# Optimization experiments

Measured on AMD Instinct MI355X. Metric: run time of the kernel, lower is better.

## Reference

```python
import jax, jax.numpy as jnp
import numpy as np

D = 256   # feature_dim
NQ = 512  # num query keypoints
NK = 512  # num key/value keypoints


def setup_inputs() -> dict:
    key = jax.random.key(0)
    ks = jax.random.split(key, 10)
    def w(k, shape, fan_in):
        return jax.random.normal(k, shape, dtype=jnp.float32) / np.sqrt(fan_in)
    inp = {
        "x": jax.random.normal(ks[0], (1, D, NQ), dtype=jnp.float32),
        "source": jax.random.normal(ks[1], (1, D, NK), dtype=jnp.float32),
        # MLPAttention score MLP: Conv1d(2D->D,k=1), ReLU, Conv1d(D->1,k=1)
        "w1": w(ks[2], (D, 2 * D), 2 * D),
        "b1": w(ks[3], (D,), 2 * D),
        "w2": w(ks[4], (1, D), D),
        "b2": w(ks[5], (1,), D),
        # outer MLP: Conv1d(2D->2D,k=1), ReLU, Conv1d(2D->D,k=1) with zero bias init
        "wa": w(ks[6], (2 * D, 2 * D), 2 * D),
        "ba": w(ks[7], (2 * D,), 2 * D),
        "wb": w(ks[8], (D, 2 * D), 2 * D),
        "bb": jnp.zeros((D,), dtype=jnp.float32),
    }
    return inp


def reference(x, source, w1, b1, w2, b2, wa, ba, wb, bb):
    d = x.shape[1]
    q = x[0]       # [D, nq]
    k = source[0]  # [D, nk]
    # cat((q broadcast over nk, k broadcast over nq)) then Conv1d(2D->D) is
    # equivalent to splitting w1 into query/key halves and broadcasting:
    w1q, w1k = w1[:, :d], w1[:, d:]
    aq = w1q @ q + b1[:, None]                       # [D, nq]
    ak = w1k @ k                                     # [D, nk]
    h = jax.nn.relu(aq[:, :, None] + ak[:, None, :])  # [D, nq, nk]
    scores = (jnp.einsum('d,dnm->nm', w2[0], h) + b2[0])[None]  # [1, nq, nk]
    prob = jax.nn.softmax(scores, axis=-1)
    message = jnp.einsum('bnm,bdm->bdn', prob, source)  # [1, D, nq]
    # outer MLP on cat([x, message], channel dim)
    cat = jnp.concatenate([x, message], axis=1)         # [1, 2D, nq]
    h2 = jax.nn.relu(jnp.einsum('oc,bcn->bon', wa, cat) + ba[None, :, None])
    y = jnp.einsum('oc,bcn->bon', wb, h2) + bb[None, :, None]  # [1, D, nq]
    return (y, scores)
```

## Files before the change

kernel.cpp:

```cpp
#include <hip/hip_runtime.h>
#include <hip/hip_bf16.h>

#define DD 256
#define NN 512

typedef __attribute__((ext_vector_type(8))) short short8;
typedef __attribute__((ext_vector_type(4))) float floatx4;

__device__ __forceinline__ unsigned short f2bf(float f) {
  unsigned u = __float_as_uint(f);
  u += 0x7FFFu + ((u >> 16) & 1u);
  return (unsigned short)(u >> 16);
}
__device__ __forceinline__ unsigned pack2(float a, float b) {
  return (unsigned)f2bf(a) | ((unsigned)f2bf(b) << 16);
}
__device__ __forceinline__ float bflo(unsigned u) { return __uint_as_float(u << 16); }
__device__ __forceinline__ float bfhi(unsigned u) { return __uint_as_float(u & 0xFFFF0000u); }

__device__ __forceinline__ short8 ldfrag(const unsigned short* __restrict__ base,
                                         int row, int ld, int k, int lane) {
  return *(const short8*)(base + (row + (lane & 15)) * ld + k + ((lane >> 4) << 3));
}

template <int NF>
__device__ __forceinline__ void acc_zero(floatx4 acc[NF]) {
#pragma unroll
  for (int i = 0; i < NF; ++i) {
    acc[i][0] = 0.f; acc[i][1] = 0.f; acc[i][2] = 0.f; acc[i][3] = 0.f;
  }
}

template <int NF>
__device__ __forceinline__ void ksplit_combine(floatx4 acc[NF], float* red,
                                               int wave, int lane) {
  const int W = 16 * NF;
  const int col = lane & 15;
  const int q = lane >> 4;
  if (wave > 0) {
    float* base = red + (wave - 1) * 16 * W;
#pragma unroll
    for (int nf = 0; nf < NF; ++nf)
#pragma unroll
      for (int r = 0; r < 4; ++r)
        base[(q * 4 + r) * W + nf * 16 + col] = acc[nf][r];
  }
  __syncthreads();
  if (wave == 0) {
#pragma unroll
    for (int nf = 0; nf < NF; ++nf)
#pragma unroll
      for (int r = 0; r < 4; ++r) {
        const int idx = (q * 4 + r) * W + nf * 16 + col;
        acc[nf][r] += red[idx] + red[16 * W + idx] + red[32 * W + idx];
      }
  }
}

template <int NF, bool COLBIAS, bool ROWBIAS, bool RELU, bool OUTBF>
__device__ __forceinline__ void gemm_epi(floatx4 acc[NF],
    const float* __restrict__ bias, void* __restrict__ C, int ldc,
    int m0, int n0, int lane) {
  const int col = lane & 15;
  const int q = lane >> 4;
#pragma unroll
  for (int nf = 0; nf < NF; ++nf) {
    const int n = n0 + nf * 16 + col;
    const float cb = COLBIAS ? bias[n] : 0.0f;
#pragma unroll
    for (int r = 0; r < 4; ++r) {
      const int m = m0 + q * 4 + r;
      float v = acc[nf][r] + cb + (ROWBIAS ? bias[m] : 0.0f);
      if (RELU) v = fmaxf(v, 0.0f);
      if (OUTBF) ((unsigned short*)C)[m * ldc + n] = f2bf(v);
      else       ((float*)C)[m * ldc + n] = v;
    }
  }
}

__global__ __launch_bounds__(256) void prep_kernel(
    const float* __restrict__ x, const float* __restrict__ src,
    const float* __restrict__ w1, const float* __restrict__ wa,
    const float* __restrict__ wb, const float* __restrict__ bb,
    unsigned short* __restrict__ w1b, unsigned short* __restrict__ wab,
    unsigned short* __restrict__ wbb, unsigned short* __restrict__ srcb,
    unsigned short* __restrict__ xT, unsigned short* __restrict__ srcT,
    float* __restrict__ y) {
  const int bid = blockIdx.x;
  const int tid = threadIdx.x;
  if (bid < 640) {
    const float* in; unsigned short* out; int off;
    if (bid < 128)      { in = w1;  out = w1b; off = bid; }
    else if (bid < 384) { in = wa;  out = wab; off = bid - 128; }
    else if (bid < 512) { in = wb;  out = wbb; off = bid - 384; }
    else                { in = src; out = srcb; off = bid - 512; }
    const int i = off * 1024 + tid * 4;
    const float4 v = *(const float4*)(in + i);
    *(uint2*)(out + i) = make_uint2(pack2(v.x, v.y), pack2(v.z, v.w));
  } else if (bid < 896) {
    __shared__ float tile[32][33];
    const int b = bid - 640;
    const float* in = (b >> 7) ? src : x;
    unsigned short* out = (b >> 7) ? srcT : xT;
    const int t = b & 127;
    const int n0 = (t >> 3) * 32;
    const int d0 = (t & 7) * 32;
    const int tx = tid & 31, ty = tid >> 5;
#pragma unroll
    for (int i = ty; i < 32; i += 8)
      tile[i][tx] = in[(d0 + i) * NN + n0 + tx];
    __syncthreads();
#pragma unroll
    for (int i = ty; i < 32; i += 8)
      out[(n0 + i) * DD + d0 + tx] = f2bf(tile[tx][i]);
  } else {
    const int i = (bid - 896) * 1024 + tid * 4;
    const float bv = bb[i >> 9];
    float4 o; o.x = bv; o.y = bv; o.z = bv; o.w = bv;
    *(float4*)(y + i) = o;
  }
}

__global__ __launch_bounds__(256) void qks_kernel(
    const unsigned short* __restrict__ w1b, const unsigned short* __restrict__ xT,
    const unsigned short* __restrict__ srcT, const float* __restrict__ b1,
    const float* __restrict__ w2, const float* __restrict__ b2,
    float* __restrict__ sc) {
  __shared__ __align__(16) unsigned short aqs[256][36];
  __shared__ __align__(16) unsigned short aks[256][36];
  __shared__ __align__(16) float part[4][32][32];
  __shared__ float w2s[DD];

  const int tid = threadIdx.x;
  const int lane = tid & 63;
  const int wave = tid >> 6;
  const int n0 = blockIdx.x * 32;
  const int m0 = blockIdx.y * 32;

  w2s[tid] = w2[tid];

  {
    const int col = lane & 15, q = lane >> 4;
#pragma unroll
    for (int j = 0; j < 8; ++j) {
      const int jid = wave * 8 + j;
      const int z = jid >> 4;
      const int d0t = (jid & 15) * 16;
      const unsigned short* BT = z ? srcT : xT;
      const int tok0 = z ? m0 : n0;
      floatx4 acc[2]; acc_zero<2>(acc);
#pragma unroll
      for (int kc = 0; kc < 8; ++kc) {
        const int c0 = kc * 32;
        short8 a = ldfrag(w1b, d0t, NN, z * 256 + c0, lane);
#pragma unroll
        for (int nf = 0; nf < 2; ++nf) {
          short8 b = ldfrag(BT, tok0 + nf * 16, DD, c0, lane);
          acc[nf] = __builtin_amdgcn_mfma_f32_16x16x32_bf16(a, b, acc[nf], 0, 0, 0);
        }
      }
#pragma unroll
      for (int nf = 0; nf < 2; ++nf)
#pragma unroll
        for (int r = 0; r < 4; ++r) {
          const int d = d0t + q * 4 + r;
          float v = acc[nf][r] + (z ? 0.0f : b1[d]);
          (z ? aks : aqs)[d][nf * 16 + col] = f2bf(v);
        }
    }
  }
  __syncthreads();

  {
    const int nq = lane & 7;
    const int mq = lane >> 3;
    float s[4][4];
#pragma unroll
    for (int i = 0; i < 4; ++i)
#pragma unroll
      for (int j = 0; j < 4; ++j) s[i][j] = 0.f;

    const int dbeg = wave * 64;
    for (int dd = dbeg; dd < dbeg + 64; ++dd) {
      const uint2 aw = *(const uint2*)&aqs[dd][nq * 4];
      const uint2 kw = *(const uint2*)&aks[dd][mq * 4];
      const float w = w2s[dd];
      float a[4] = {bflo(aw.x), bfhi(aw.x), bflo(aw.y), bfhi(aw.y)};
      float k[4] = {bflo(kw.x), bfhi(kw.x), bflo(kw.y), bfhi(kw.y)};
#pragma unroll
      for (int i = 0; i < 4; ++i)
#pragma unroll
        for (int j = 0; j < 4; ++j)
          s[i][j] += w * fmaxf(a[i] + k[j], 0.f);
    }
#pragma unroll
    for (int i = 0; i < 4; ++i)
#pragma unroll
      for (int j = 0; j < 4; ++j)
        part[wave][nq * 4 + i][mq * 4 + j] = s[i][j];
  }
  __syncthreads();

  {
    const int n = tid >> 3;
    const int mg = (tid & 7) * 4;
    float4 p0 = *(const float4*)&part[0][n][mg];
    float4 p1 = *(const float4*)&part[1][n][mg];
    float4 p2 = *(const float4*)&part[2][n][mg];
    float4 p3 = *(const float4*)&part[3][n][mg];
    const float bv = b2[0];
    float4 o;
    o.x = p0.x + p1.x + p2.x + p3.x + bv;
    o.y = p0.y + p1.y + p2.y + p3.y + bv;
    o.z = p0.z + p1.z + p2.z + p3.z + bv;
    o.w = p0.w + p1.w + p2.w + p3.w + bv;
    *(float4*)&sc[(n0 + n) * NN + m0 + mg] = o;
  }
}

__global__ __launch_bounds__(256) void msgT_kernel(
    const float* __restrict__ sc, const unsigned short* __restrict__ srcb,
    unsigned short* __restrict__ msgTb) {
  __shared__ unsigned short Ap[16][520];
  __shared__ float red[1536];
  __shared__ float smax[16][16];
  __shared__ float ssum[16][16];
  __shared__ float rst[16][2];

  const int tid = threadIdx.x;
  const int lane = tid & 63;
  const int wave = tid >> 6;
  const int n0 = blockIdx.y * 16;
  const int d0 = blockIdx.x * 32;

  const int r = tid >> 4;
  const int c = tid & 15;
  float4 v[8];
  const float* rp = sc + (n0 + r) * NN + c * 4;
#pragma unroll
  for (int i = 0; i < 8; ++i) v[i] = *(const float4*)(rp + i * 64);

  float mx = -3.0e38f;
#pragma unroll
  for (int i = 0; i < 8; ++i)
    mx = fmaxf(mx, fmaxf(fmaxf(v[i].x, v[i].y), fmaxf(v[i].z, v[i].w)));
  smax[r][c] = mx;
  __syncthreads();
  if (c == 0) {
    float m2 = smax[r][0];
#pragma unroll
    for (int i = 1; i < 16; ++i) m2 = fmaxf(m2, smax[r][i]);
    rst[r][0] = m2;
  }
  __syncthreads();
  mx = rst[r][0];

  float sum = 0.f;
#pragma unroll
  for (int i = 0; i < 8; ++i) {
    v[i].x = __expf(v[i].x - mx); v[i].y = __expf(v[i].y - mx);
    v[i].z = __expf(v[i].z - mx); v[i].w = __expf(v[i].w - mx);
    sum += v[i].x + v[i].y + v[i].z + v[i].w;
  }
  ssum[r][c] = sum;
  __syncthreads();
  if (c == 0) {
    float s2 = ssum[r][0];
#pragma unroll
    for (int i = 1; i < 16; ++i) s2 += ssum[r][i];
    rst[r][1] = s2;
  }
  __syncthreads();
  const float inv = 1.0f / rst[r][1];
#pragma unroll
  for (int i = 0; i < 8; ++i) {
    *(unsigned*)&Ap[r][c * 4 + i * 64]     = pack2(v[i].x * inv, v[i].y * inv);
    *(unsigned*)&Ap[r][c * 4 + i * 64 + 2] = pack2(v[i].z * inv, v[i].w * inv);
  }
  __syncthreads();

  floatx4 acc[2]; acc_zero<2>(acc);
  const int k0w = wave * 128;
  const int arow = lane & 15;
  const int koff = (lane >> 4) << 3;
#pragma unroll
  for (int k = 0; k < 128; k += 32) {
    short8 a = *(const short8*)&Ap[arow][k0w + k + koff];
#pragma unroll
    for (int nf = 0; nf < 2; ++nf) {
      short8 b = ldfrag(srcb, d0 + nf * 16, NN, k0w + k, lane);
      acc[nf] = __builtin_amdgcn_mfma_f32_16x16x32_bf16(a, b, acc[nf], 0, 0, 0);
    }
  }
  ksplit_combine<2>(acc, red, wave, lane);
  if (wave == 0)
    gemm_epi<2, false, false, false, true>(acc, nullptr, msgTb, DD, n0, d0, lane);
}

__global__ __launch_bounds__(256) void h2y_kernel(
    const unsigned short* __restrict__ xT, const unsigned short* __restrict__ msgTb,
    const unsigned short* __restrict__ wab, const unsigned short* __restrict__ wbb,
    const float* __restrict__ ba, float* __restrict__ y) {
  __shared__ __align__(16) unsigned short h2L[16][144];

  const int tid = threadIdx.x;
  const int lane = tid & 63;
  const int wave = tid >> 6;
  const int nt = blockIdx.x >> 2;
  const int qh = blockIdx.x & 3;
  const int n0g = nt * 16;
  const int o0 = qh * 128;

  {
    floatx4 acc[2]; acc_zero<2>(acc);
    const int ow = o0 + wave * 32;
#pragma unroll
    for (int kc = 0; kc < 16; ++kc) {
      const int c0 = kc * 32;
      short8 a = (c0 < 256) ? ldfrag(xT, n0g, DD, c0, lane)
                            : ldfrag(msgTb, n0g, DD, c0 - 256, lane);
#pragma unroll
      for (int nf = 0; nf < 2; ++nf) {
        short8 b = ldfrag(wab, ow + nf * 16, NN, c0, lane);
        acc[nf] = __builtin_amdgcn_mfma_f32_16x16x32_bf16(a, b, acc[nf], 0, 0, 0);
      }
    }
    const int col = lane & 15, q = lane >> 4;
#pragma unroll
    for (int nf = 0; nf < 2; ++nf) {
      const int ol = wave * 32 + nf * 16 + col;
      const float cb = ba[o0 + ol];
#pragma unroll
      for (int r = 0; r < 4; ++r)
        h2L[q * 4 + r][ol] = f2bf(fmaxf(acc[nf][r] + cb, 0.f));
    }
  }
  __syncthreads();

  {
    const int brow = lane & 15;
    const int koff = (lane >> 4) << 3;
    const int col = lane & 15, q = lane >> 4;
#pragma unroll
    for (int t = 0; t < 4; ++t) {
      const int o2t = wave * 64 + t * 16;
      floatx4 acc;
      acc[0] = 0.f; acc[1] = 0.f; acc[2] = 0.f; acc[3] = 0.f;
#pragma unroll
      for (int kc = 0; kc < 4; ++kc) {
        short8 a = ldfrag(wbb, o2t, NN, o0 + kc * 32, lane);
        short8 b = *(const short8*)&h2L[brow][kc * 32 + koff];
        acc = __builtin_amdgcn_mfma_f32_16x16x32_bf16(a, b, acc, 0, 0, 0);
      }
#pragma unroll
      for (int r = 0; r < 4; ++r)
        atomicAdd(&y[(o2t + q * 4 + r) * NN + n0g + col], acc[r]);
    }
  }
}

extern "C" void kernel_launch(void* const* d_in, const int* in_sizes, int n_in,
                              void* d_out, int out_size, void* d_ws, size_t ws_size,
                              hipStream_t stream) {
  (void)in_sizes; (void)n_in; (void)out_size; (void)ws_size;

  const float* x   = (const float*)d_in[0];
  const float* src = (const float*)d_in[1];
  const float* w1  = (const float*)d_in[2];
  const float* b1  = (const float*)d_in[3];
  const float* w2  = (const float*)d_in[4];
  const float* b2  = (const float*)d_in[5];
  const float* wa  = (const float*)d_in[6];
  const float* ba  = (const float*)d_in[7];
  const float* wb  = (const float*)d_in[8];
  const float* bb  = (const float*)d_in[9];

  float* y_out  = (float*)d_out;
  float* sc_out = (float*)d_out + 131072;

  char* ws = (char*)d_ws;
  unsigned short* w1b   = (unsigned short*)(ws);
  unsigned short* wab   = (unsigned short*)(ws + (256 << 10));
  unsigned short* wbb   = (unsigned short*)(ws + (768 << 10));
  unsigned short* srcb  = (unsigned short*)(ws + (1024 << 10));
  unsigned short* xT    = (unsigned short*)(ws + (1280 << 10));
  unsigned short* srcT  = (unsigned short*)(ws + (1536 << 10));
  unsigned short* msgTb = (unsigned short*)(ws + (1792 << 10));

  prep_kernel<<<1024, 256, 0, stream>>>(x, src, w1, wa, wb, bb,
                                        w1b, wab, wbb, srcb, xT, srcT, y_out);
  qks_kernel<<<dim3(16, 16), 256, 0, stream>>>(w1b, xT, srcT, b1, w2, b2, sc_out);
  msgT_kernel<<<dim3(8, 32), 256, 0, stream>>>(sc_out, srcb, msgTb);
  h2y_kernel<<<128, 256, 0, stream>>>(xT, msgTb, wab, wbb, ba, y_out);
}
```

Measured before the change: 122.7 us.

## Drop bf16 prep pass; convert fp32 inputs on the fly and split aq/ak from scores

Removes the separate prep kernel that converted weights and inputs to bf16 and transposed them. The GEMM kernels now read fp32 directly and convert to bf16 in registers (ldfrag_f32), or transpose through LDS. aq/ak are now computed once by a dedicated kernel into fp32 workspace instead of being recomputed per score tile, and the scores kernel reads them back. The aim is to cut redundant aq/ak recomputation and the extra conversion traffic. In exchange, the weights are re-read and re-converted in fp32 by many blocks, which means more global bytes per fragment and strided LDS transposes.

```diff
diff --git a/kernel.cpp b/kernel.cpp
--- a/kernel.cpp
+++ b/kernel.cpp
@@ -15,12 +15,33 @@
 __device__ __forceinline__ unsigned pack2(float a, float b) {
   return (unsigned)f2bf(a) | ((unsigned)f2bf(b) << 16);
 }
-__device__ __forceinline__ float bflo(unsigned u) { return __uint_as_float(u << 16); }
-__device__ __forceinline__ float bfhi(unsigned u) { return __uint_as_float(u & 0xFFFF0000u); }
 
 __device__ __forceinline__ short8 ldfrag(const unsigned short* __restrict__ base,
                                          int row, int ld, int k, int lane) {
   return *(const short8*)(base + (row + (lane & 15)) * ld + k + ((lane >> 4) << 3));
+}
+
+__device__ __forceinline__ short8 ldfrag_f32(const float* __restrict__ base,
+                                             int row, int ld, int k, int lane) {
+  const float* p = base + (row + (lane & 15)) * ld + k + ((lane >> 4) << 3);
+  const float4 v0 = *(const float4*)p;
+  const float4 v1 = *(const float4*)(p + 4);
+  short8 r;
+  r[0] = (short)f2bf(v0.x); r[1] = (short)f2bf(v0.y);
+  r[2] = (short)f2bf(v0.z); r[3] = (short)f2bf(v0.w);
+  r[4] = (short)f2bf(v1.x); r[5] = (short)f2bf(v1.y);
+  r[6] = (short)f2bf(v1.z); r[7] = (short)f2bf(v1.w);
+  return r;
+}
+
+__device__ __forceinline__ short8 ldfragT_lds(const float* __restrict__ xs, int ldxs,
+                                              int nrow, int k, int lane) {
+  const int n = nrow + (lane & 15);
+  const int kk = k + ((lane >> 4) << 3);
+  short8 r;
+#pragma unroll
+  for (int j = 0; j < 8; ++j) r[j] = (short)f2bf(xs[(kk + j) * ldxs + n]);
+  return r;
 }
 
 template <int NF>
@@ -78,148 +99,103 @@
   }
 }
 
-__global__ __launch_bounds__(256) void prep_kernel(
+__global__ __launch_bounds__(256) void aqak_kernel(
     const float* __restrict__ x, const float* __restrict__ src,
-    const float* __restrict__ w1, const float* __restrict__ wa,
-    const float* __restrict__ wb, const float* __restrict__ bb,
-    unsigned short* __restrict__ w1b, unsigned short* __restrict__ wab,
-    unsigned short* __restrict__ wbb, unsigned short* __restrict__ srcb,
-    unsigned short* __restrict__ xT, unsigned short* __restrict__ srcT,
-    float* __restrict__ y) {
-  const int bid = blockIdx.x;
+    const float* __restrict__ w1, const float* __restrict__ b1,
+    const float* __restrict__ bb,
+    float* __restrict__ aq, float* __restrict__ ak, float* __restrict__ y) {
+  __shared__ float xs[256][33];
+  __shared__ float red[1536];
+
   const int tid = threadIdx.x;
-  if (bid < 640) {
-    const float* in; unsigned short* out; int off;
-    if (bid < 128)      { in = w1;  out = w1b; off = bid; }
-    else if (bid < 384) { in = wa;  out = wab; off = bid - 128; }
-    else if (bid < 512) { in = wb;  out = wbb; off = bid - 384; }
-    else                { in = src; out = srcb; off = bid - 512; }
-    const int i = off * 1024 + tid * 4;
-    const float4 v = *(const float4*)(in + i);
-    *(uint2*)(out + i) = make_uint2(pack2(v.x, v.y), pack2(v.z, v.w));
-  } else if (bid < 896) {
-    __shared__ float tile[32][33];
-    const int b = bid - 640;
-    const float* in = (b >> 7) ? src : x;
-    unsigned short* out = (b >> 7) ? srcT : xT;
-    const int t = b & 127;
-    const int n0 = (t >> 3) * 32;
-    const int d0 = (t & 7) * 32;
-    const int tx = tid & 31, ty = tid >> 5;
-#pragma unroll
-    for (int i = ty; i < 32; i += 8)
-      tile[i][tx] = in[(d0 + i) * NN + n0 + tx];
-    __syncthreads();
-#pragma unroll
-    for (int i = ty; i < 32; i += 8)
-      out[(n0 + i) * DD + d0 + tx] = f2bf(tile[tx][i]);
-  } else {
-    const int i = (bid - 896) * 1024 + tid * 4;
-    const float bv = bb[i >> 9];
-    float4 o; o.x = bv; o.y = bv; o.z = bv; o.w = bv;
-    *(float4*)(y + i) = o;
-  }
-}
-
-__global__ __launch_bounds__(256) void qks_kernel(
-    const unsigned short* __restrict__ w1b, const unsigned short* __restrict__ xT,
-    const unsigned short* __restrict__ srcT, const float* __restrict__ b1,
+  const int z = blockIdx.z;
+
+  if (z == 2) {
+    const int o = blockIdx.y * 16 + blockIdx.x;
+    const float bv = bb[o];
+    float2 v; v.x = bv; v.y = bv;
+    *(float2*)&y[o * NN + tid * 2] = v;
+    return;
+  }
+
+  const int lane = tid & 63;
+  const int wave = tid >> 6;
+  const int m0 = blockIdx.y * 16;
+  const int n0 = blockIdx.x * 32;
+  const float* in = z ? src : x;
+
+#pragma unroll
+  for (int p = 0; p < 8; ++p) {
+    const int d = p * 32 + (tid >> 3);
+    const int c4 = (tid & 7) * 4;
+    const float4 v = *(const float4*)&in[d * NN + n0 + c4];
+    xs[d][c4 + 0] = v.x; xs[d][c4 + 1] = v.y;
+    xs[d][c4 + 2] = v.z; xs[d][c4 + 3] = v.w;
+  }
+  __syncthreads();
+
+  floatx4 acc[2]; acc_zero<2>(acc);
+#pragma unroll
+  for (int kc = 0; kc < 2; ++kc) {
+    const int kl = wave * 64 + kc * 32;
+    short8 a = ldfrag_f32(w1, m0, NN, z * 256 + kl, lane);
+#pragma unroll
+    for (int nf = 0; nf < 2; ++nf) {
+      short8 b = ldfragT_lds(&xs[0][0], 33, nf * 16, kl, lane);
+      acc[nf] = __builtin_amdgcn_mfma_f32_16x16x32_bf16(a, b, acc[nf], 0, 0, 0);
+    }
+  }
+  ksplit_combine<2>(acc, red, wave, lane);
+  if (wave == 0) {
+    if (z == 0) gemm_epi<2, false, true, false, false>(acc, b1, aq, NN, m0, n0, lane);
+    else        gemm_epi<2, false, false, false, false>(acc, nullptr, ak, NN, m0, n0, lane);
+  }
+}
+
+__global__ __launch_bounds__(256) void scores_kernel(
+    const float* __restrict__ aq, const float* __restrict__ ak,
     const float* __restrict__ w2, const float* __restrict__ b2,
     float* __restrict__ sc) {
-  __shared__ __align__(16) unsigned short aqs[256][36];
-  __shared__ __align__(16) unsigned short aks[256][36];
-  __shared__ __align__(16) float part[4][32][32];
+  __shared__ float aqs[128][32];
+  __shared__ float aks[128][32];
   __shared__ float w2s[DD];
 
   const int tid = threadIdx.x;
-  const int lane = tid & 63;
-  const int wave = tid >> 6;
   const int n0 = blockIdx.x * 32;
   const int m0 = blockIdx.y * 32;
+  const int tn = tid & 31;
+  const int tm4 = (tid >> 5) * 4;
 
   w2s[tid] = w2[tid];
 
-  {
-    const int col = lane & 15, q = lane >> 4;
-#pragma unroll
-    for (int j = 0; j < 8; ++j) {
-      const int jid = wave * 8 + j;
-      const int z = jid >> 4;
-      const int d0t = (jid & 15) * 16;
-      const unsigned short* BT = z ? srcT : xT;
-      const int tok0 = z ? m0 : n0;
-      floatx4 acc[2]; acc_zero<2>(acc);
-#pragma unroll
-      for (int kc = 0; kc < 8; ++kc) {
-        const int c0 = kc * 32;
-        short8 a = ldfrag(w1b, d0t, NN, z * 256 + c0, lane);
-#pragma unroll
-        for (int nf = 0; nf < 2; ++nf) {
-          short8 b = ldfrag(BT, tok0 + nf * 16, DD, c0, lane);
-          acc[nf] = __builtin_amdgcn_mfma_f32_16x16x32_bf16(a, b, acc[nf], 0, 0, 0);
-        }
-      }
-#pragma unroll
-      for (int nf = 0; nf < 2; ++nf)
-#pragma unroll
-        for (int r = 0; r < 4; ++r) {
-          const int d = d0t + q * 4 + r;
-          float v = acc[nf][r] + (z ? 0.0f : b1[d]);
-          (z ? aks : aqs)[d][nf * 16 + col] = f2bf(v);
-        }
-    }
-  }
-  __syncthreads();
-
-  {
-    const int nq = lane & 7;
-    const int mq = lane >> 3;
-    float s[4][4];
-#pragma unroll
-    for (int i = 0; i < 4; ++i)
-#pragma unroll
-      for (int j = 0; j < 4; ++j) s[i][j] = 0.f;
-
-    const int dbeg = wave * 64;
-    for (int dd = dbeg; dd < dbeg + 64; ++dd) {
-      const uint2 aw = *(const uint2*)&aqs[dd][nq * 4];
-      const uint2 kw = *(const uint2*)&aks[dd][mq * 4];
-      const float w = w2s[dd];
-      float a[4] = {bflo(aw.x), bfhi(aw.x), bflo(aw.y), bfhi(aw.y)};
-      float k[4] = {bflo(kw.x), bfhi(kw.x), bflo(kw.y), bfhi(kw.y)};
-#pragma unroll
-      for (int i = 0; i < 4; ++i)
-#pragma unroll
-        for (int j = 0; j < 4; ++j)
-          s[i][j] += w * fmaxf(a[i] + k[j], 0.f);
-    }
-#pragma unroll
-    for (int i = 0; i < 4; ++i)
-#pragma unroll
-      for (int j = 0; j < 4; ++j)
-        part[wave][nq * 4 + i][mq * 4 + j] = s[i][j];
-  }
-  __syncthreads();
-
-  {
-    const int n = tid >> 3;
-    const int mg = (tid & 7) * 4;
-    float4 p0 = *(const float4*)&part[0][n][mg];
-    float4 p1 = *(const float4*)&part[1][n][mg];
-    float4 p2 = *(const float4*)&part[2][n][mg];
-    float4 p3 = *(const float4*)&part[3][n][mg];
-    const float bv = b2[0];
-    float4 o;
-    o.x = p0.x + p1.x + p2.x + p3.x + bv;
-    o.y = p0.y + p1.y + p2.y + p3.y + bv;
-    o.z = p0.z + p1.z + p2.z + p3.z + bv;
-    o.w = p0.w + p1.w + p2.w + p3.w + bv;
-    *(float4*)&sc[(n0 + n) * NN + m0 + mg] = o;
-  }
+  float s0 = 0.f, s1 = 0.f, s2 = 0.f, s3 = 0.f;
+  for (int d0 = 0; d0 < DD; d0 += 128) {
+    __syncthreads();
+#pragma unroll
+    for (int k = 0; k < 16; ++k) {
+      const int idx = k * 256 + tid;
+      const int r = idx >> 5, cc = idx & 31;
+      aqs[r][cc] = aq[(d0 + r) * NN + n0 + cc];
+      aks[r][cc] = ak[(d0 + r) * NN + m0 + cc];
+    }
+    __syncthreads();
+    for (int dd = 0; dd < 128; ++dd) {
+      const float w = w2s[d0 + dd];
+      const float a = aqs[dd][tn];
+      const float4 akv = *(const float4*)&aks[dd][tm4];
+      s0 += w * fmaxf(a + akv.x, 0.f);
+      s1 += w * fmaxf(a + akv.y, 0.f);
+      s2 += w * fmaxf(a + akv.z, 0.f);
+      s3 += w * fmaxf(a + akv.w, 0.f);
+    }
+  }
+  const float bv = b2[0];
+  float4 o; o.x = s0 + bv; o.y = s1 + bv; o.z = s2 + bv; o.w = s3 + bv;
+  *(float4*)&sc[(n0 + tn) * NN + m0 + tm4] = o;
 }
 
 __global__ __launch_bounds__(256) void msgT_kernel(
-    const float* __restrict__ sc, const unsigned short* __restrict__ srcb,
+    const float* __restrict__ sc, const float* __restrict__ srcf,
     unsigned short* __restrict__ msgTb) {
   __shared__ unsigned short Ap[16][520];
   __shared__ float red[1536];
@@ -288,7 +264,7 @@
     short8 a = *(const short8*)&Ap[arow][k0w + k + koff];
 #pragma unroll
     for (int nf = 0; nf < 2; ++nf) {
-      short8 b = ldfrag(srcb, d0 + nf * 16, NN, k0w + k, lane);
+      short8 b = ldfrag_f32(srcf, d0 + nf * 16, NN, k0w + k, lane);
       acc[nf] = __builtin_amdgcn_mfma_f32_16x16x32_bf16(a, b, acc[nf], 0, 0, 0);
     }
   }
@@ -298,10 +274,11 @@
 }
 
 __global__ __launch_bounds__(256) void h2y_kernel(
-    const unsigned short* __restrict__ xT, const unsigned short* __restrict__ msgTb,
-    const unsigned short* __restrict__ wab, const unsigned short* __restrict__ wbb,
+    const float* __restrict__ x, const unsigned short* __restrict__ msgTb,
+    const float* __restrict__ waf, const float* __restrict__ wbf,
     const float* __restrict__ ba, float* __restrict__ y) {
-  __shared__ __align__(16) unsigned short h2L[16][144];
+  __shared__ float xs[256][17];
+  __shared__ __align__(16) unsigned short h2L[16][152];
 
   const int tid = threadIdx.x;
   const int lane = tid & 63;
@@ -311,17 +288,25 @@
   const int n0g = nt * 16;
   const int o0 = qh * 128;
 
+#pragma unroll
+  for (int p = 0; p < 16; ++p) {
+    const int d = p * 16 + (tid >> 4);
+    const int n = tid & 15;
+    xs[d][n] = x[d * NN + n0g + n];
+  }
+  __syncthreads();
+
   {
     floatx4 acc[2]; acc_zero<2>(acc);
     const int ow = o0 + wave * 32;
 #pragma unroll
     for (int kc = 0; kc < 16; ++kc) {
       const int c0 = kc * 32;
-      short8 a = (c0 < 256) ? ldfrag(xT, n0g, DD, c0, lane)
+      short8 a = (c0 < 256) ? ldfragT_lds(&xs[0][0], 17, 0, c0, lane)
                             : ldfrag(msgTb, n0g, DD, c0 - 256, lane);
 #pragma unroll
       for (int nf = 0; nf < 2; ++nf) {
-        short8 b = ldfrag(wab, ow + nf * 16, NN, c0, lane);
+        short8 b = ldfrag_f32(waf, ow + nf * 16, NN, c0, lane);
         acc[nf] = __builtin_amdgcn_mfma_f32_16x16x32_bf16(a, b, acc[nf], 0, 0, 0);
       }
     }
@@ -348,7 +333,7 @@
       acc[0] = 0.f; acc[1] = 0.f; acc[2] = 0.f; acc[3] = 0.f;
 #pragma unroll
       for (int kc = 0; kc < 4; ++kc) {
-        short8 a = ldfrag(wbb, o2t, NN, o0 + kc * 32, lane);
+        short8 a = ldfrag_f32(wbf, o2t, NN, o0 + kc * 32, lane);
         short8 b = *(const short8*)&h2L[brow][kc * 32 + koff];
         acc = __builtin_amdgcn_mfma_f32_16x16x32_bf16(a, b, acc, 0, 0, 0);
       }
@@ -379,17 +364,12 @@
   float* sc_out = (float*)d_out + 131072;
 
   char* ws = (char*)d_ws;
-  unsigned short* w1b   = (unsigned short*)(ws);
-  unsigned short* wab   = (unsigned short*)(ws + (256 << 10));
-  unsigned short* wbb   = (unsigned short*)(ws + (768 << 10));
-  unsigned short* srcb  = (unsigned short*)(ws + (1024 << 10));
-  unsigned short* xT    = (unsigned short*)(ws + (1280 << 10));
-  unsigned short* srcT  = (unsigned short*)(ws + (1536 << 10));
-  unsigned short* msgTb = (unsigned short*)(ws + (1792 << 10));
-
-  prep_kernel<<<1024, 256, 0, stream>>>(x, src, w1, wa, wb, bb,
-                                        w1b, wab, wbb, srcb, xT, srcT, y_out);
-  qks_kernel<<<dim3(16, 16), 256, 0, stream>>>(w1b, xT, srcT, b1, w2, b2, sc_out);
-  msgT_kernel<<<dim3(8, 32), 256, 0, stream>>>(sc_out, srcb, msgTb);
-  h2y_kernel<<<128, 256, 0, stream>>>(xT, msgTb, wab, wbb, ba, y_out);
-}
+  float*          aq    = (float*)(ws);
+  float*          ak    = (float*)(ws + (512 << 10));
+  unsigned short* msgTb = (unsigned short*)(ws + (1024 << 10));
+
+  aqak_kernel<<<dim3(16, 16, 3), 256, 0, stream>>>(x, src, w1, b1, bb, aq, ak, y_out);
+  scores_kernel<<<dim3(16, 16), 256, 0, stream>>>(aq, ak, w2, b2, sc_out);
+  msgT_kernel<<<dim3(8, 32), 256, 0, stream>>>(sc_out, src, msgTb);
+  h2y_kernel<<<128, 256, 0, stream>>>(x, msgTb, wa, wb, ba, y_out);
+}
```

Result: faster. 108.0 us (-12.0%).
